# Performance work log

Hardware: AMD Instinct MI355X
Metric: run time of the kernel (lower is better)

Reference implementation:

```python
import jax, jax.numpy as jnp
import numpy as np

N, E, D, H, OUT = 50000, 640000, 128, 128, 32


def setup_inputs() -> dict:
    key = jax.random.key(0)
    ks = jax.random.split(key, 12)
    s = 0.02
    return {
        "x": jax.random.normal(ks[0], (N, D), dtype=jnp.float32),
        "edge_src": jax.random.randint(ks[1], (E,), 0, N),
        "edge_dst": jax.random.randint(ks[2], (E,), 0, N),
        "Wp": jax.random.normal(ks[3], (D, H), dtype=jnp.float32) * s,
        "bp": jnp.zeros((H,), jnp.float32),
        "Wm": jax.random.normal(ks[4], (2 * H, H), dtype=jnp.float32) * s,
        "bm": jnp.zeros((H,), jnp.float32),
        "Wu": jax.random.normal(ks[5], (2 * H, H), dtype=jnp.float32) * s,
        "bu": jnp.zeros((H,), jnp.float32),
        "gamma": jnp.ones((H,), jnp.float32),
        "beta": jnp.zeros((H,), jnp.float32),
        "Wd": jax.random.normal(ks[6], (H, OUT), dtype=jnp.float32) * s,
        "bd": jnp.zeros((OUT,), jnp.float32),
    }


def reference(x, edge_src, edge_dst, Wp, bp, Wm, bm, Wu, bu, gamma, beta, Wd, bd):
    n = x.shape[0]
    h = H
    # node projection: [N, H]
    h0 = x @ Wp + bp
    # edge messages: relu(concat(h0[src], h0[dst]) @ Wm + bm), split matmul avoids concat
    msg = jax.nn.relu(h0[edge_src] @ Wm[:h] + h0[edge_dst] @ Wm[h:] + bm)  # [E, H]
    # segment-mean into target nodes
    pooled_sum = jax.ops.segment_sum(msg, edge_dst, num_segments=n)
    cnt = jax.ops.segment_sum(jnp.ones((msg.shape[0],), msg.dtype), edge_dst, num_segments=n)
    pooled = pooled_sum / jnp.maximum(cnt, 1.0)[:, None]  # [N, H]
    # residual next-state: relu(h0 + Dense(concat(h0, pooled)))
    upd = h0 @ Wu[:h] + pooled @ Wu[h:] + bu
    hn = jax.nn.relu(h0 + upd)
    # layer norm over feature axis
    mu = jnp.mean(hn, axis=-1, keepdims=True)
    var = jnp.mean(jnp.square(hn - mu), axis=-1, keepdims=True)
    hn = (hn - mu) * jax.lax.rsqrt(var + 1e-6) * gamma + beta
    # graph-level mean pool -> [1, H] -> [1, OUT]
    g = jnp.mean(hn, axis=0, keepdims=True)
    return g @ Wd + bd
```

## Files before the change

kernel.cpp:

```cpp
#include <hip/hip_runtime.h>

#define N_NODES 50000
#define N_EDGES 640000
#define HD 128
#define TILE_N 128
#define NSCB 196

typedef short bf16x8 __attribute__((ext_vector_type(8)));
typedef float f32x4 __attribute__((ext_vector_type(4)));
typedef unsigned short u16x8 __attribute__((ext_vector_type(8)));
typedef unsigned short u16x4 __attribute__((ext_vector_type(4)));

__device__ __forceinline__ unsigned short f2bf(float f) {
  unsigned u = __float_as_uint(f);
  return (unsigned short)((u + 0x7fffu + ((u >> 16) & 1u)) >> 16);
}
__device__ __forceinline__ float bf2f(unsigned short h) {
  return __uint_as_float(((unsigned)h) << 16);
}
__device__ __forceinline__ int swzb(int row, int u) {
  return row * 256 + ((u ^ (row & 7)) << 4);
}

__device__ __forceinline__ void load_A(const char* Ash, int lane, int wr, bf16x8 A[4][4]) {
  const int l15 = lane & 15, l4 = lane >> 4;
#pragma unroll
  for (int rt = 0; rt < 4; ++rt)
#pragma unroll
    for (int kk = 0; kk < 4; ++kk)
      A[rt][kk] = *(const bf16x8*)(Ash + swzb(wr * 64 + rt * 16 + l15, kk * 4 + l4));
}

__device__ __forceinline__ void mfma_AB(const bf16x8 A[4][4], const char* Bsh,
                                        int lane, int wc, f32x4 acc[4][4]) {
  const int l15 = lane & 15, l4 = lane >> 4;
#pragma unroll
  for (int ct = 0; ct < 4; ++ct) {
    bf16x8 B[4];
#pragma unroll
    for (int kk = 0; kk < 4; ++kk)
      B[kk] = *(const bf16x8*)(Bsh + swzb(wc * 64 + ct * 16 + l15, kk * 4 + l4));
#pragma unroll
    for (int rt = 0; rt < 4; ++rt)
#pragma unroll
      for (int kk = 0; kk < 4; ++kk)
        acc[rt][ct] =
            __builtin_amdgcn_mfma_f32_16x16x32_bf16(A[rt][kk], B[kk], acc[rt][ct], 0, 0, 0);
  }
}

__device__ __forceinline__ void scatter_acc(char* Tsh, int lane, int wr, int wc,
                                            const f32x4 acc[4][4]) {
  const int l15 = lane & 15, l4 = lane >> 4;
#pragma unroll
  for (int rt = 0; rt < 4; ++rt)
#pragma unroll
    for (int ct = 0; ct < 4; ++ct) {
      int c = wc * 64 + ct * 16 + l15;
#pragma unroll
      for (int e = 0; e < 4; ++e) {
        int r = wr * 64 + rt * 16 + l4 * 4 + e;
        *(unsigned short*)(Tsh + swzb(r, c >> 3) + (c & 7) * 2) = f2bf(acc[rt][ct][e]);
      }
    }
}

__device__ __forceinline__ void copy_out(const char* Tsh, unsigned short* __restrict__ g,
                                         int bnode0, int tid) {
#pragma unroll
  for (int c = 0; c < 8; ++c) {
    int ul = c * 256 + tid;
    int row = ul >> 4, u = ul & 15;
    if (bnode0 + row < N_NODES)
      *(u16x8*)(g + (size_t)(bnode0 + row) * HD + u * 8) = *(const u16x8*)(Tsh + swzb(row, u));
  }
}

__device__ __forceinline__ void stage_bf(const unsigned short* __restrict__ src, char* Tsh,
                                         int bnode0, int tid, bool guard) {
#pragma unroll
  for (int c = 0; c < 8; ++c) {
    int ul = c * 256 + tid;
    int row = ul >> 4, u = ul & 15;
    u16x8 v = {0, 0, 0, 0, 0, 0, 0, 0};
    if (!guard || (bnode0 + row < N_NODES))
      v = *(const u16x8*)(src + (size_t)(bnode0 + row) * HD + u * 8);
    *(u16x8*)(Tsh + swzb(row, u)) = v;
  }
}

__device__ __forceinline__ void stage_xf(const float* __restrict__ src, char* Tsh,
                                         int bnode0, int tid) {
#pragma unroll
  for (int c = 0; c < 16; ++c) {
    int f4 = c * 256 + tid;
    int row = f4 >> 5, c4 = f4 & 31;
    float4 v = make_float4(0.f, 0.f, 0.f, 0.f);
    if (bnode0 + row < N_NODES) v = ((const float4*)src)[(size_t)(bnode0 + row) * 32 + c4];
    u16x4 p;
    p[0] = f2bf(v.x); p[1] = f2bf(v.y); p[2] = f2bf(v.z); p[3] = f2bf(v.w);
    *(u16x4*)(Tsh + swzb(row, c4 >> 1) + (c4 & 1) * 8) = p;
  }
}

__global__ __launch_bounds__(128) void k_prew(const float* __restrict__ Wp,
                                              const float* __restrict__ Wm,
                                              const float* __restrict__ Wu,
                                              unsigned short* __restrict__ WT) {
  const int s = blockIdx.x;
  const float* src = (s == 0) ? Wp : (s == 1) ? Wm : (s == 2) ? (Wm + HD * HD)
                     : (s == 3) ? Wu : (Wu + HD * HD);
  const int n = threadIdx.x;
  unsigned short* dst = WT + (size_t)s * HD * HD + (size_t)n * HD;
  for (int kc = 0; kc < HD; kc += 8) {
    u16x8 p;
#pragma unroll
    for (int j = 0; j < 8; ++j) p[j] = f2bf(src[(size_t)(kc + j) * HD + n]);
    *(u16x8*)(dst + kc) = p;
  }
}

__global__ __launch_bounds__(256, 2) void k_proj(
    const float* __restrict__ x, const unsigned short* __restrict__ WT,
    const float* __restrict__ bp, const float* __restrict__ bm,
    unsigned short* __restrict__ h0, unsigned short* __restrict__ a,
    unsigned short* __restrict__ b) {
  __shared__ char Ssh[32768];
  __shared__ char Wsh[32768];
  const int tid = threadIdx.x, lane = tid & 63, wid = tid >> 6;
  const int wr = wid >> 1, wc = wid & 1, l15 = lane & 15;
  const int bnode0 = blockIdx.x * TILE_N;

  stage_xf(x, Ssh, bnode0, tid);
  stage_bf(WT, Wsh, 0, tid, false);
  __syncthreads();

  bf16x8 A[4][4];
  f32x4 acc[4][4];
  load_A(Ssh, lane, wr, A);
#pragma unroll
  for (int ct = 0; ct < 4; ++ct) {
    float bv = bp[wc * 64 + ct * 16 + l15];
    f32x4 sv = {bv, bv, bv, bv};
#pragma unroll
    for (int rt = 0; rt < 4; ++rt) acc[rt][ct] = sv;
  }
  mfma_AB(A, Wsh, lane, wc, acc);
  __syncthreads();
  scatter_acc(Ssh, lane, wr, wc, acc);
  stage_bf(WT + 1 * HD * HD, Wsh, 0, tid, false);
  __syncthreads();
  copy_out(Ssh, h0, bnode0, tid);
  load_A(Ssh, lane, wr, A);
#pragma unroll
  for (int ct = 0; ct < 4; ++ct) {
    f32x4 z = {0.f, 0.f, 0.f, 0.f};
#pragma unroll
    for (int rt = 0; rt < 4; ++rt) acc[rt][ct] = z;
  }
  mfma_AB(A, Wsh, lane, wc, acc);
  __syncthreads();
  scatter_acc(Ssh, lane, wr, wc, acc);
  stage_bf(WT + 2 * HD * HD, Wsh, 0, tid, false);
  __syncthreads();
  copy_out(Ssh, a, bnode0, tid);
#pragma unroll
  for (int ct = 0; ct < 4; ++ct) {
    float bv = bm[wc * 64 + ct * 16 + l15];
    f32x4 sv = {bv, bv, bv, bv};
#pragma unroll
    for (int rt = 0; rt < 4; ++rt) acc[rt][ct] = sv;
  }
  mfma_AB(A, Wsh, lane, wc, acc);
  __syncthreads();
  scatter_acc(Ssh, lane, wr, wc, acc);
  __syncthreads();
  copy_out(Ssh, b, bnode0, tid);
}

__global__ void k_hist(const int* __restrict__ dst, int* __restrict__ deg,
                       int* __restrict__ pos_e) {
  int e = blockIdx.x * 256 + threadIdx.x;
  if (e < N_EDGES) pos_e[e] = atomicAdd(&deg[dst[e]], 1);
}

__global__ __launch_bounds__(256) void k_scan1(const int* __restrict__ deg,
                                               int* __restrict__ bsum) {
  __shared__ int sh[256];
  int i = blockIdx.x * 256 + threadIdx.x;
  sh[threadIdx.x] = (i < N_NODES) ? deg[i] : 0;
  __syncthreads();
  for (int off = 128; off > 0; off >>= 1) {
    if (threadIdx.x < off) sh[threadIdx.x] += sh[threadIdx.x + off];
    __syncthreads();
  }
  if (threadIdx.x == 0) bsum[blockIdx.x] = sh[0];
}

__global__ __launch_bounds__(256) void k_scan2(const int* __restrict__ bsum,
                                               int* __restrict__ boff,
                                               int* __restrict__ row_start) {
  __shared__ int sh[256];
  int t = threadIdx.x;
  int v = (t < NSCB) ? bsum[t] : 0;
  sh[t] = v;
  __syncthreads();
  for (int off = 1; off < 256; off <<= 1) {
    int add = (t >= off) ? sh[t - off] : 0;
    __syncthreads();
    sh[t] += add;
    __syncthreads();
  }
  if (t < NSCB) boff[t] = sh[t] - v;
  if (t == 255) row_start[N_NODES] = sh[255];
}

__global__ __launch_bounds__(256) void k_scan3(const int* __restrict__ deg,
                                               const int* __restrict__ boff,
                                               int* __restrict__ row_start) {
  __shared__ int sh[256];
  int t = threadIdx.x;
  int i = blockIdx.x * 256 + t;
  int v = (i < N_NODES) ? deg[i] : 0;
  sh[t] = v;
  __syncthreads();
  for (int off = 1; off < 256; off <<= 1) {
    int add = (t >= off) ? sh[t - off] : 0;
    __syncthreads();
    sh[t] += add;
    __syncthreads();
  }
  if (i < N_NODES) row_start[i] = boff[blockIdx.x] + sh[t] - v;
}

__global__ void k_scatter(const int* __restrict__ src, const int* __restrict__ dst,
                          const int* __restrict__ pos_e, const int* __restrict__ row_start,
                          int* __restrict__ es) {
  int e = blockIdx.x * 256 + threadIdx.x;
  if (e < N_EDGES) {
    int d = dst[e];
    es[row_start[d] + pos_e[e]] = src[e];
  }
}

__global__ __launch_bounds__(256) void k_agg(const unsigned short* __restrict__ a,
                                             const unsigned short* __restrict__ b,
                                             const int* __restrict__ es,
                                             const int* __restrict__ row_start,
                                             unsigned short* __restrict__ pooled) {
  const int node = blockIdx.x * 4 + (threadIdx.x >> 6);
  const int lane = threadIdx.x & 63;
  const int s = row_start[node];
  const int e = row_start[node + 1];
  const unsigned bu = ((const unsigned*)(b + (size_t)node * HD))[lane];
  const float bx = bf2f((unsigned short)(bu & 0xffffu));
  const float by = bf2f((unsigned short)(bu >> 16));
  float ax = 0.f, ay = 0.f;
  int i = s;
  for (; i + 8 <= e; i += 8) {
    unsigned av[8];
#pragma unroll
    for (int j = 0; j < 8; ++j)
      av[j] = ((const unsigned*)(a + (size_t)es[i + j] * HD))[lane];
#pragma unroll
    for (int j = 0; j < 8; ++j) {
      ax += fmaxf(bf2f((unsigned short)(av[j] & 0xffffu)) + bx, 0.f);
      ay += fmaxf(bf2f((unsigned short)(av[j] >> 16)) + by, 0.f);
    }
  }
  for (; i + 4 <= e; i += 4) {
    unsigned av[4];
#pragma unroll
    for (int j = 0; j < 4; ++j)
      av[j] = ((const unsigned*)(a + (size_t)es[i + j] * HD))[lane];
#pragma unroll
    for (int j = 0; j < 4; ++j) {
      ax += fmaxf(bf2f((unsigned short)(av[j] & 0xffffu)) + bx, 0.f);
      ay += fmaxf(bf2f((unsigned short)(av[j] >> 16)) + by, 0.f);
    }
  }
  for (; i < e; ++i) {
    unsigned a0 = ((const unsigned*)(a + (size_t)es[i] * HD))[lane];
    ax += fmaxf(bf2f((unsigned short)(a0 & 0xffffu)) + bx, 0.f);
    ay += fmaxf(bf2f((unsigned short)(a0 >> 16)) + by, 0.f);
  }
  const float inv = 1.f / fmaxf((float)(e - s), 1.f);
  unsigned o = (unsigned)f2bf(ax * inv) | ((unsigned)f2bf(ay * inv) << 16);
  ((unsigned*)(pooled + (size_t)node * HD))[lane] = o;
}

__global__ __launch_bounds__(256, 2) void k_upd(
    const unsigned short* __restrict__ h0, const unsigned short* __restrict__ pooled,
    const unsigned short* __restrict__ WT, const float* __restrict__ bu,
    const float* __restrict__ gamma, const float* __restrict__ beta,
    float* __restrict__ gsum) {
  __shared__ char Ssh[32768];
  __shared__ char Wsh[32768];
  const int tid = threadIdx.x, lane = tid & 63, wid = tid >> 6;
  const int wr = wid >> 1, wc = wid & 1, l15 = lane & 15, l4 = lane >> 4;
  const int bnode0 = blockIdx.x * TILE_N;

  stage_bf(pooled, Ssh, bnode0, tid, true);
  stage_bf(WT + 4 * HD * HD, Wsh, 0, tid, false);
  __syncthreads();

  bf16x8 A[4][4];
  f32x4 acc[4][4];
  load_A(Ssh, lane, wr, A);
#pragma unroll
  for (int ct = 0; ct < 4; ++ct) {
    float bv = bu[wc * 64 + ct * 16 + l15];
    f32x4 sv = {bv, bv, bv, bv};
#pragma unroll
    for (int rt = 0; rt < 4; ++rt) acc[rt][ct] = sv;
  }
  mfma_AB(A, Wsh, lane, wc, acc);
  __syncthreads();
  stage_bf(h0, Ssh, bnode0, tid, true);
  stage_bf(WT + 3 * HD * HD, Wsh, 0, tid, false);
  __syncthreads();
  load_A(Ssh, lane, wr, A);
  mfma_AB(A, Wsh, lane, wc, acc);
  __syncthreads();

  float rsum[4][4], rsq[4][4];
#pragma unroll
  for (int rt = 0; rt < 4; ++rt)
#pragma unroll
    for (int e = 0; e < 4; ++e) {
      int r = wr * 64 + rt * 16 + l4 * 4 + e;
      float srow = 0.f, qrow = 0.f;
#pragma unroll
      for (int ct = 0; ct < 4; ++ct) {
        int c = wc * 64 + ct * 16 + l15;
        float hv = bf2f(*(const unsigned short*)(Ssh + swzb(r, c >> 3) + (c & 7) * 2));
        float v = fmaxf(hv + acc[rt][ct][e], 0.f);
        acc[rt][ct][e] = v;
        srow += v;
        qrow += v * v;
      }
#pragma unroll
      for (int m = 1; m < 16; m <<= 1) {
        srow += __shfl_xor(srow, m);
        qrow += __shfl_xor(qrow, m);
      }
      rsum[rt][e] = srow;
      rsq[rt][e] = qrow;
    }
  float* pS = (float*)Wsh;
  float* pQ = (float*)(Wsh + 1024);
  if (l15 == 0) {
#pragma unroll
    for (int rt = 0; rt < 4; ++rt)
#pragma unroll
      for (int e = 0; e < 4; ++e) {
        int r = wr * 64 + rt * 16 + l4 * 4 + e;
        pS[r * 2 + wc] = rsum[rt][e];
        pQ[r * 2 + wc] = rsq[rt][e];
      }
  }
  __syncthreads();

  float g4[4], b4[4];
#pragma unroll
  for (int ct = 0; ct < 4; ++ct) {
    int c = wc * 64 + ct * 16 + l15;
    g4[ct] = gamma[c];
    b4[ct] = beta[c];
  }
  float gp[4] = {0.f, 0.f, 0.f, 0.f};
#pragma unroll
  for (int rt = 0; rt < 4; ++rt)
#pragma unroll
    for (int e = 0; e < 4; ++e) {
      int r = wr * 64 + rt * 16 + l4 * 4 + e;
      float s = pS[r * 2] + pS[r * 2 + 1];
      float q = pQ[r * 2] + pQ[r * 2 + 1];
      float mu = s * (1.f / 128.f);
      float var = q * (1.f / 128.f) - mu * mu;
      float rs = rsqrtf(var + 1e-6f);
      bool valid = (bnode0 + r) < N_NODES;
#pragma unroll
      for (int ct = 0; ct < 4; ++ct) {
        float v = (acc[rt][ct][e] - mu) * rs * g4[ct] + b4[ct];
        if (valid) gp[ct] += v;
      }
    }
#pragma unroll
  for (int ct = 0; ct < 4; ++ct) {
    gp[ct] += __shfl_xor(gp[ct], 16);
    gp[ct] += __shfl_xor(gp[ct], 32);
  }
  if (lane < 16) {
#pragma unroll
    for (int ct = 0; ct < 4; ++ct) atomicAdd(&gsum[wc * 64 + ct * 16 + lane], gp[ct]);
  }
}

__global__ void k_final(const float* __restrict__ gsum, const float* __restrict__ Wd,
                        const float* __restrict__ bd, float* __restrict__ out) {
  int o = threadIdx.x;
  if (o < 32) {
    float acc = bd[o];
    const float invN = 1.f / (float)N_NODES;
    for (int d = 0; d < HD; ++d) acc = fmaf(gsum[d] * invN, Wd[d * 32 + o], acc);
    out[o] = acc;
  }
}

extern "C" void kernel_launch(void* const* d_in, const int* in_sizes, int n_in,
                              void* d_out, int out_size, void* d_ws, size_t ws_size,
                              hipStream_t stream) {
  (void)in_sizes; (void)n_in; (void)out_size; (void)ws_size;
  const float* x    = (const float*)d_in[0];
  const int* esrc   = (const int*)d_in[1];
  const int* edst   = (const int*)d_in[2];
  const float* Wp   = (const float*)d_in[3];
  const float* bp   = (const float*)d_in[4];
  const float* Wm   = (const float*)d_in[5];
  const float* bm   = (const float*)d_in[6];
  const float* Wu   = (const float*)d_in[7];
  const float* bu   = (const float*)d_in[8];
  const float* gam  = (const float*)d_in[9];
  const float* bet  = (const float*)d_in[10];
  const float* Wd   = (const float*)d_in[11];
  const float* bd   = (const float*)d_in[12];
  float* out = (float*)d_out;

  char* ws = (char*)d_ws;
  size_t off = 0;
  unsigned short* WT     = (unsigned short*)(ws + off); off += 5 * (size_t)HD * HD * 2;
  unsigned short* h0     = (unsigned short*)(ws + off); off += (size_t)N_NODES * HD * 2;
  unsigned short* a      = (unsigned short*)(ws + off); off += (size_t)N_NODES * HD * 2;
  unsigned short* b      = (unsigned short*)(ws + off); off += (size_t)N_NODES * HD * 2;
  unsigned short* pooled = (unsigned short*)(ws + off); off += (size_t)N_NODES * HD * 2;
  int* es        = (int*)(ws + off);   off += (size_t)N_EDGES * 4;
  int* pos_e     = (int*)(ws + off);   off += (size_t)N_EDGES * 4;
  int* deg       = (int*)(ws + off);   off += (size_t)N_NODES * 4;
  float* gsum    = (float*)(ws + off); off += 128 * 4;
  int* row_start = (int*)(ws + off);   off += (size_t)(N_NODES + 1) * 4;
  int* bsum      = (int*)(ws + off);   off += (size_t)NSCB * 4;
  int* boff      = (int*)(ws + off);   off += (size_t)NSCB * 4;

  hipMemsetAsync(deg, 0, (size_t)(N_NODES + 128) * 4, stream);
  k_prew<<<5, 128, 0, stream>>>(Wp, Wm, Wu, WT);
  k_proj<<<(N_NODES + TILE_N - 1) / TILE_N, 256, 0, stream>>>(x, WT, bp, bm, h0, a, b);
  k_hist<<<(N_EDGES + 255) / 256, 256, 0, stream>>>(edst, deg, pos_e);
  k_scan1<<<NSCB, 256, 0, stream>>>(deg, bsum);
  k_scan2<<<1, 256, 0, stream>>>(bsum, boff, row_start);
  k_scan3<<<NSCB, 256, 0, stream>>>(deg, boff, row_start);
  k_scatter<<<(N_EDGES + 255) / 256, 256, 0, stream>>>(esrc, edst, pos_e, row_start, es);
  k_agg<<<N_NODES / 4, 256, 0, stream>>>(a, b, es, row_start, pooled);
  k_upd<<<(N_NODES + TILE_N - 1) / TILE_N, 256, 0, stream>>>(h0, pooled, WT, bu, gam, bet, gsum);
  k_final<<<1, 64, 0, stream>>>(gsum, Wd, bd, out);
}
```

Measured before the change: 222.3 us.

## Fuse neighbor aggregation into update kernel and fold final dense into last block

Gathers and mean-pools edge messages straight into shared memory inside the update kernel, which removes the pooled buffer's global round trip and one launch. The final small dense layer now runs in whichever block finishes last, detected with an atomic counter, and the memset is folded into the weight-prep kernel by adding zeroing blocks. The cost is parallelism in aggregation: each block now handles 128 nodes with 4 waves, one node per wave at a time, against 12500 small blocks before. That may hurt latency hiding for the random gathers.

```diff
diff --git a/kernel.cpp b/kernel.cpp
--- a/kernel.cpp
+++ b/kernel.cpp
@@ -5,6 +5,7 @@
 #define HD 128
 #define TILE_N 128
 #define NSCB 196
+#define NTILE 391
 
 typedef short bf16x8 __attribute__((ext_vector_type(8)));
 typedef float f32x4 __attribute__((ext_vector_type(4)));
@@ -106,7 +107,13 @@
 __global__ __launch_bounds__(128) void k_prew(const float* __restrict__ Wp,
                                               const float* __restrict__ Wm,
                                               const float* __restrict__ Wu,
-                                              unsigned short* __restrict__ WT) {
+                                              unsigned short* __restrict__ WT,
+                                              int* __restrict__ zbase) {
+  if (blockIdx.x >= 5) {
+    int idx = (blockIdx.x - 5) * 512 + threadIdx.x * 4;
+    *(int4*)(zbase + idx) = make_int4(0, 0, 0, 0);
+    return;
+  }
   const int s = blockIdx.x;
   const float* src = (s == 0) ? Wp : (s == 1) ? Wm : (s == 2) ? (Wm + HD * HD)
                      : (s == 3) ? Wu : (Wu + HD * HD);
@@ -243,65 +250,63 @@
   }
 }
 
-__global__ __launch_bounds__(256) void k_agg(const unsigned short* __restrict__ a,
-                                             const unsigned short* __restrict__ b,
-                                             const int* __restrict__ es,
-                                             const int* __restrict__ row_start,
-                                             unsigned short* __restrict__ pooled) {
-  const int node = blockIdx.x * 4 + (threadIdx.x >> 6);
-  const int lane = threadIdx.x & 63;
-  const int s = row_start[node];
-  const int e = row_start[node + 1];
-  const unsigned bu = ((const unsigned*)(b + (size_t)node * HD))[lane];
-  const float bx = bf2f((unsigned short)(bu & 0xffffu));
-  const float by = bf2f((unsigned short)(bu >> 16));
-  float ax = 0.f, ay = 0.f;
-  int i = s;
-  for (; i + 8 <= e; i += 8) {
-    unsigned av[8];
-#pragma unroll
-    for (int j = 0; j < 8; ++j)
-      av[j] = ((const unsigned*)(a + (size_t)es[i + j] * HD))[lane];
-#pragma unroll
-    for (int j = 0; j < 8; ++j) {
-      ax += fmaxf(bf2f((unsigned short)(av[j] & 0xffffu)) + bx, 0.f);
-      ay += fmaxf(bf2f((unsigned short)(av[j] >> 16)) + by, 0.f);
-    }
-  }
-  for (; i + 4 <= e; i += 4) {
-    unsigned av[4];
-#pragma unroll
-    for (int j = 0; j < 4; ++j)
-      av[j] = ((const unsigned*)(a + (size_t)es[i + j] * HD))[lane];
-#pragma unroll
-    for (int j = 0; j < 4; ++j) {
-      ax += fmaxf(bf2f((unsigned short)(av[j] & 0xffffu)) + bx, 0.f);
-      ay += fmaxf(bf2f((unsigned short)(av[j] >> 16)) + by, 0.f);
-    }
-  }
-  for (; i < e; ++i) {
-    unsigned a0 = ((const unsigned*)(a + (size_t)es[i] * HD))[lane];
-    ax += fmaxf(bf2f((unsigned short)(a0 & 0xffffu)) + bx, 0.f);
-    ay += fmaxf(bf2f((unsigned short)(a0 >> 16)) + by, 0.f);
-  }
-  const float inv = 1.f / fmaxf((float)(e - s), 1.f);
-  unsigned o = (unsigned)f2bf(ax * inv) | ((unsigned)f2bf(ay * inv) << 16);
-  ((unsigned*)(pooled + (size_t)node * HD))[lane] = o;
-}
-
-__global__ __launch_bounds__(256, 2) void k_upd(
-    const unsigned short* __restrict__ h0, const unsigned short* __restrict__ pooled,
-    const unsigned short* __restrict__ WT, const float* __restrict__ bu,
-    const float* __restrict__ gamma, const float* __restrict__ beta,
-    float* __restrict__ gsum) {
+__global__ __launch_bounds__(256, 2) void k_aggupd(
+    const unsigned short* __restrict__ h0, const unsigned short* __restrict__ a,
+    const unsigned short* __restrict__ b, const int* __restrict__ es,
+    const int* __restrict__ row_start, const unsigned short* __restrict__ WT,
+    const float* __restrict__ bu, const float* __restrict__ gamma,
+    const float* __restrict__ beta, const float* __restrict__ Wd,
+    const float* __restrict__ bd, float* __restrict__ gsum,
+    int* __restrict__ done, float* __restrict__ out) {
   __shared__ char Ssh[32768];
   __shared__ char Wsh[32768];
+  __shared__ int lastflag;
   const int tid = threadIdx.x, lane = tid & 63, wid = tid >> 6;
   const int wr = wid >> 1, wc = wid & 1, l15 = lane & 15, l4 = lane >> 4;
   const int bnode0 = blockIdx.x * TILE_N;
 
-  stage_bf(pooled, Ssh, bnode0, tid, true);
   stage_bf(WT + 4 * HD * HD, Wsh, 0, tid, false);
+  for (int rr = 0; rr < 32; ++rr) {
+    const int row = wid * 32 + rr;
+    const int n = bnode0 + row;
+    unsigned packed = 0;
+    if (n < N_NODES) {
+      const int s = row_start[n];
+      const int e = row_start[n + 1];
+      const unsigned bv = ((const unsigned*)(b + (size_t)n * HD))[lane];
+      const float bx = bf2f((unsigned short)(bv & 0xffffu));
+      const float by = bf2f((unsigned short)(bv >> 16));
+      float ax = 0.f, ay = 0.f;
+      int i = s;
+      for (; i + 8 <= e; i += 8) {
+        unsigned av[8];
+#pragma unroll
+        for (int j = 0; j < 8; ++j)
+          av[j] = ((const unsigned*)(a + (size_t)es[i + j] * HD))[lane];
+#pragma unroll
+        for (int j = 0; j < 8; ++j) {
+          ax += fmaxf(bf2f((unsigned short)(av[j] & 0xffffu)) + bx, 0.f);
+          ay += fmaxf(bf2f((unsigned short)(av[j] >> 16)) + by, 0.f);
+        }
+      }
+      for (; i + 2 <= e; i += 2) {
+        unsigned a0 = ((const unsigned*)(a + (size_t)es[i] * HD))[lane];
+        unsigned a1 = ((const unsigned*)(a + (size_t)es[i + 1] * HD))[lane];
+        ax += fmaxf(bf2f((unsigned short)(a0 & 0xffffu)) + bx, 0.f);
+        ay += fmaxf(bf2f((unsigned short)(a0 >> 16)) + by, 0.f);
+        ax += fmaxf(bf2f((unsigned short)(a1 & 0xffffu)) + bx, 0.f);
+        ay += fmaxf(bf2f((unsigned short)(a1 >> 16)) + by, 0.f);
+      }
+      for (; i < e; ++i) {
+        unsigned a0 = ((const unsigned*)(a + (size_t)es[i] * HD))[lane];
+        ax += fmaxf(bf2f((unsigned short)(a0 & 0xffffu)) + bx, 0.f);
+        ay += fmaxf(bf2f((unsigned short)(a0 >> 16)) + by, 0.f);
+      }
+      const float inv = 1.f / fmaxf((float)(e - s), 1.f);
+      packed = (unsigned)f2bf(ax * inv) | ((unsigned)f2bf(ay * inv) << 16);
+    }
+    *(unsigned*)(Ssh + swzb(row, lane >> 2) + (lane & 3) * 4) = packed;
+  }
   __syncthreads();
 
   bf16x8 A[4][4];
@@ -395,16 +400,19 @@
 #pragma unroll
     for (int ct = 0; ct < 4; ++ct) atomicAdd(&gsum[wc * 64 + ct * 16 + lane], gp[ct]);
   }
-}
-
-__global__ void k_final(const float* __restrict__ gsum, const float* __restrict__ Wd,
-                        const float* __restrict__ bd, float* __restrict__ out) {
-  int o = threadIdx.x;
-  if (o < 32) {
-    float acc = bd[o];
-    const float invN = 1.f / (float)N_NODES;
-    for (int d = 0; d < HD; ++d) acc = fmaf(gsum[d] * invN, Wd[d * 32 + o], acc);
-    out[o] = acc;
+
+  __threadfence();
+  __syncthreads();
+  if (tid == 0) lastflag = (atomicAdd(done, 1) == gridDim.x - 1) ? 1 : 0;
+  __syncthreads();
+  if (lastflag) {
+    __threadfence();
+    if (tid < 32) {
+      float acc2 = bd[tid];
+      const float invN = 1.f / (float)N_NODES;
+      for (int d = 0; d < HD; ++d) acc2 = fmaf(gsum[d] * invN, Wd[d * 32 + tid], acc2);
+      out[tid] = acc2;
+    }
   }
 }
 
@@ -429,28 +437,28 @@
 
   char* ws = (char*)d_ws;
   size_t off = 0;
-  unsigned short* WT     = (unsigned short*)(ws + off); off += 5 * (size_t)HD * HD * 2;
-  unsigned short* h0     = (unsigned short*)(ws + off); off += (size_t)N_NODES * HD * 2;
-  unsigned short* a      = (unsigned short*)(ws + off); off += (size_t)N_NODES * HD * 2;
-  unsigned short* b      = (unsigned short*)(ws + off); off += (size_t)N_NODES * HD * 2;
-  unsigned short* pooled = (unsigned short*)(ws + off); off += (size_t)N_NODES * HD * 2;
-  int* es        = (int*)(ws + off);   off += (size_t)N_EDGES * 4;
-  int* pos_e     = (int*)(ws + off);   off += (size_t)N_EDGES * 4;
-  int* deg       = (int*)(ws + off);   off += (size_t)N_NODES * 4;
-  float* gsum    = (float*)(ws + off); off += 128 * 4;
-  int* row_start = (int*)(ws + off);   off += (size_t)(N_NODES + 1) * 4;
-  int* bsum      = (int*)(ws + off);   off += (size_t)NSCB * 4;
-  int* boff      = (int*)(ws + off);   off += (size_t)NSCB * 4;
-
-  hipMemsetAsync(deg, 0, (size_t)(N_NODES + 128) * 4, stream);
-  k_prew<<<5, 128, 0, stream>>>(Wp, Wm, Wu, WT);
-  k_proj<<<(N_NODES + TILE_N - 1) / TILE_N, 256, 0, stream>>>(x, WT, bp, bm, h0, a, b);
+  unsigned short* WT = (unsigned short*)(ws + off); off += 5 * (size_t)HD * HD * 2;
+  unsigned short* h0 = (unsigned short*)(ws + off); off += (size_t)N_NODES * HD * 2;
+  unsigned short* a  = (unsigned short*)(ws + off); off += (size_t)N_NODES * HD * 2;
+  unsigned short* b  = (unsigned short*)(ws + off); off += (size_t)N_NODES * HD * 2;
+  int* es    = (int*)(ws + off); off += (size_t)N_EDGES * 4;
+  int* pos_e = (int*)(ws + off); off += (size_t)N_EDGES * 4;
+  int* zbase = (int*)(ws + off);
+  int* deg   = zbase;
+  float* gsum = (float*)(zbase + N_NODES);
+  int* done  = zbase + N_NODES + 128;
+  off += (size_t)50176 * 4;
+  int* row_start = (int*)(ws + off); off += (size_t)(N_NODES + 1) * 4;
+  int* bsum = (int*)(ws + off); off += (size_t)NSCB * 4;
+  int* boff = (int*)(ws + off); off += (size_t)NSCB * 4;
+
+  k_prew<<<103, 128, 0, stream>>>(Wp, Wm, Wu, WT, zbase);
+  k_proj<<<NTILE, 256, 0, stream>>>(x, WT, bp, bm, h0, a, b);
   k_hist<<<(N_EDGES + 255) / 256, 256, 0, stream>>>(edst, deg, pos_e);
   k_scan1<<<NSCB, 256, 0, stream>>>(deg, bsum);
   k_scan2<<<1, 256, 0, stream>>>(bsum, boff, row_start);
   k_scan3<<<NSCB, 256, 0, stream>>>(deg, boff, row_start);
   k_scatter<<<(N_EDGES + 255) / 256, 256, 0, stream>>>(esrc, edst, pos_e, row_start, es);
-  k_agg<<<N_NODES / 4, 256, 0, stream>>>(a, b, es, row_start, pooled);
-  k_upd<<<(N_NODES + TILE_N - 1) / TILE_N, 256, 0, stream>>>(h0, pooled, WT, bu, gam, bet, gsum);
-  k_final<<<1, 64, 0, stream>>>(gsum, Wd, bd, out);
-}
+  k_aggupd<<<NTILE, 256, 0, stream>>>(h0, a, b, es, row_start, WT, bu, gam, bet,
+                                      Wd, bd, gsum, done, out);
+}
```

After: 284.3 us. 27.9% more time.

## Cut kernel launches by merging memset, histogram, scans and final reduction

Applied to the files above, without the earlier changes.

Folds the workspace memset into extra blocks of the weight-prep kernel and runs the edge-degree histogram as extra blocks inside the projection kernel. It merges scan1 and scan2 through a last-block-done atomic counter, and moves the final dense readout into the last finishing block of the update kernel. The aim is to remove several small launches and their serialization gaps. In exchange it adds threadfence and atomic-counter synchronization. The histogram blocks also now compete with the projection GEMM blocks for occupancy.

```diff
diff --git a/kernel.cpp b/kernel.cpp
--- a/kernel.cpp
+++ b/kernel.cpp
@@ -5,6 +5,8 @@
 #define HD 128
 #define TILE_N 128
 #define NSCB 196
+#define NTILE 391
+#define HB 313
 
 typedef short bf16x8 __attribute__((ext_vector_type(8)));
 typedef float f32x4 __attribute__((ext_vector_type(4)));
@@ -106,7 +108,13 @@
 __global__ __launch_bounds__(128) void k_prew(const float* __restrict__ Wp,
                                               const float* __restrict__ Wm,
                                               const float* __restrict__ Wu,
-                                              unsigned short* __restrict__ WT) {
+                                              unsigned short* __restrict__ WT,
+                                              int* __restrict__ zbase) {
+  if (blockIdx.x >= 5) {
+    int idx = (blockIdx.x - 5) * 512 + threadIdx.x * 4;
+    *(int4*)(zbase + idx) = make_int4(0, 0, 0, 0);
+    return;
+  }
   const int s = blockIdx.x;
   const float* src = (s == 0) ? Wp : (s == 1) ? Wm : (s == 2) ? (Wm + HD * HD)
                      : (s == 3) ? Wu : (Wu + HD * HD);
@@ -120,16 +128,22 @@
   }
 }
 
-__global__ __launch_bounds__(256, 2) void k_proj(
+__global__ __launch_bounds__(256, 2) void k_projhist(
     const float* __restrict__ x, const unsigned short* __restrict__ WT,
     const float* __restrict__ bp, const float* __restrict__ bm,
     unsigned short* __restrict__ h0, unsigned short* __restrict__ a,
-    unsigned short* __restrict__ b) {
+    unsigned short* __restrict__ b, const int* __restrict__ edst,
+    int* __restrict__ deg, int* __restrict__ pos_e) {
   __shared__ char Ssh[32768];
   __shared__ char Wsh[32768];
+  if (blockIdx.x < HB) {
+    for (int e = blockIdx.x * 256 + threadIdx.x; e < N_EDGES; e += HB * 256)
+      pos_e[e] = atomicAdd(&deg[edst[e]], 1);
+    return;
+  }
   const int tid = threadIdx.x, lane = tid & 63, wid = tid >> 6;
   const int wr = wid >> 1, wc = wid & 1, l15 = lane & 15;
-  const int bnode0 = blockIdx.x * TILE_N;
+  const int bnode0 = (blockIdx.x - HB) * TILE_N;
 
   stage_xf(x, Ssh, bnode0, tid);
   stage_bf(WT, Wsh, 0, tid, false);
@@ -178,15 +192,13 @@
   copy_out(Ssh, b, bnode0, tid);
 }
 
-__global__ void k_hist(const int* __restrict__ dst, int* __restrict__ deg,
-                       int* __restrict__ pos_e) {
-  int e = blockIdx.x * 256 + threadIdx.x;
-  if (e < N_EDGES) pos_e[e] = atomicAdd(&deg[dst[e]], 1);
-}
-
-__global__ __launch_bounds__(256) void k_scan1(const int* __restrict__ deg,
-                                               int* __restrict__ bsum) {
+__global__ __launch_bounds__(256) void k_scan12(const int* __restrict__ deg,
+                                                int* __restrict__ bsum,
+                                                int* __restrict__ boff,
+                                                int* __restrict__ row_start,
+                                                int* __restrict__ done2) {
   __shared__ int sh[256];
+  __shared__ int amLast;
   int i = blockIdx.x * 256 + threadIdx.x;
   sh[threadIdx.x] = (i < N_NODES) ? deg[i] : 0;
   __syncthreads();
@@ -194,25 +206,27 @@
     if (threadIdx.x < off) sh[threadIdx.x] += sh[threadIdx.x + off];
     __syncthreads();
   }
-  if (threadIdx.x == 0) bsum[blockIdx.x] = sh[0];
-}
-
-__global__ __launch_bounds__(256) void k_scan2(const int* __restrict__ bsum,
-                                               int* __restrict__ boff,
-                                               int* __restrict__ row_start) {
-  __shared__ int sh[256];
-  int t = threadIdx.x;
-  int v = (t < NSCB) ? bsum[t] : 0;
-  sh[t] = v;
-  __syncthreads();
-  for (int off = 1; off < 256; off <<= 1) {
-    int add = (t >= off) ? sh[t - off] : 0;
+  if (threadIdx.x == 0) {
+    bsum[blockIdx.x] = sh[0];
+    __threadfence();
+    amLast = (atomicAdd(done2, 1) == gridDim.x - 1) ? 1 : 0;
+  }
+  __syncthreads();
+  if (amLast) {
+    __threadfence();
+    int t = threadIdx.x;
+    int v = (t < NSCB) ? bsum[t] : 0;
+    sh[t] = v;
     __syncthreads();
-    sh[t] += add;
-    __syncthreads();
-  }
-  if (t < NSCB) boff[t] = sh[t] - v;
-  if (t == 255) row_start[N_NODES] = sh[255];
+    for (int off = 1; off < 256; off <<= 1) {
+      int add = (t >= off) ? sh[t - off] : 0;
+      __syncthreads();
+      sh[t] += add;
+      __syncthreads();
+    }
+    if (t < NSCB) boff[t] = sh[t] - v;
+    if (t == 255) row_start[N_NODES] = sh[255];
+  }
 }
 
 __global__ __launch_bounds__(256) void k_scan3(const int* __restrict__ deg,
@@ -293,9 +307,11 @@
     const unsigned short* __restrict__ h0, const unsigned short* __restrict__ pooled,
     const unsigned short* __restrict__ WT, const float* __restrict__ bu,
     const float* __restrict__ gamma, const float* __restrict__ beta,
-    float* __restrict__ gsum) {
+    const float* __restrict__ Wd, const float* __restrict__ bd,
+    float* __restrict__ gsum, int* __restrict__ done, float* __restrict__ out) {
   __shared__ char Ssh[32768];
   __shared__ char Wsh[32768];
+  __shared__ int lastflag;
   const int tid = threadIdx.x, lane = tid & 63, wid = tid >> 6;
   const int wr = wid >> 1, wc = wid & 1, l15 = lane & 15, l4 = lane >> 4;
   const int bnode0 = blockIdx.x * TILE_N;
@@ -395,16 +411,19 @@
 #pragma unroll
     for (int ct = 0; ct < 4; ++ct) atomicAdd(&gsum[wc * 64 + ct * 16 + lane], gp[ct]);
   }
-}
-
-__global__ void k_final(const float* __restrict__ gsum, const float* __restrict__ Wd,
-                        const float* __restrict__ bd, float* __restrict__ out) {
-  int o = threadIdx.x;
-  if (o < 32) {
-    float acc = bd[o];
-    const float invN = 1.f / (float)N_NODES;
-    for (int d = 0; d < HD; ++d) acc = fmaf(gsum[d] * invN, Wd[d * 32 + o], acc);
-    out[o] = acc;
+
+  __threadfence();
+  __syncthreads();
+  if (tid == 0) lastflag = (atomicAdd(done, 1) == gridDim.x - 1) ? 1 : 0;
+  __syncthreads();
+  if (lastflag) {
+    __threadfence();
+    if (tid < 32) {
+      float acc2 = bd[tid];
+      const float invN = 1.f / (float)N_NODES;
+      for (int d = 0; d < HD; ++d) acc2 = fmaf(gsum[d] * invN, Wd[d * 32 + tid], acc2);
+      out[tid] = acc2;
+    }
   }
 }
 
@@ -434,23 +453,23 @@
   unsigned short* a      = (unsigned short*)(ws + off); off += (size_t)N_NODES * HD * 2;
   unsigned short* b      = (unsigned short*)(ws + off); off += (size_t)N_NODES * HD * 2;
   unsigned short* pooled = (unsigned short*)(ws + off); off += (size_t)N_NODES * HD * 2;
-  int* es        = (int*)(ws + off);   off += (size_t)N_EDGES * 4;
-  int* pos_e     = (int*)(ws + off);   off += (size_t)N_EDGES * 4;
-  int* deg       = (int*)(ws + off);   off += (size_t)N_NODES * 4;
-  float* gsum    = (float*)(ws + off); off += 128 * 4;
-  int* row_start = (int*)(ws + off);   off += (size_t)(N_NODES + 1) * 4;
-  int* bsum      = (int*)(ws + off);   off += (size_t)NSCB * 4;
-  int* boff      = (int*)(ws + off);   off += (size_t)NSCB * 4;
-
-  hipMemsetAsync(deg, 0, (size_t)(N_NODES + 128) * 4, stream);
-  k_prew<<<5, 128, 0, stream>>>(Wp, Wm, Wu, WT);
-  k_proj<<<(N_NODES + TILE_N - 1) / TILE_N, 256, 0, stream>>>(x, WT, bp, bm, h0, a, b);
-  k_hist<<<(N_EDGES + 255) / 256, 256, 0, stream>>>(edst, deg, pos_e);
-  k_scan1<<<NSCB, 256, 0, stream>>>(deg, bsum);
-  k_scan2<<<1, 256, 0, stream>>>(bsum, boff, row_start);
+  int* es    = (int*)(ws + off); off += (size_t)N_EDGES * 4;
+  int* pos_e = (int*)(ws + off); off += (size_t)N_EDGES * 4;
+  int* zbase = (int*)(ws + off);
+  int* deg   = zbase;
+  float* gsum = (float*)(zbase + N_NODES);
+  int* done  = zbase + N_NODES + 128;
+  int* done2 = zbase + N_NODES + 129;
+  off += (size_t)50176 * 4;
+  int* row_start = (int*)(ws + off); off += (size_t)(N_NODES + 1) * 4;
+  int* bsum = (int*)(ws + off); off += (size_t)NSCB * 4;
+  int* boff = (int*)(ws + off); off += (size_t)NSCB * 4;
+
+  k_prew<<<103, 128, 0, stream>>>(Wp, Wm, Wu, WT, zbase);
+  k_projhist<<<HB + NTILE, 256, 0, stream>>>(x, WT, bp, bm, h0, a, b, edst, deg, pos_e);
+  k_scan12<<<NSCB, 256, 0, stream>>>(deg, bsum, boff, row_start, done2);
   k_scan3<<<NSCB, 256, 0, stream>>>(deg, boff, row_start);
   k_scatter<<<(N_EDGES + 255) / 256, 256, 0, stream>>>(esrc, edst, pos_e, row_start, es);
   k_agg<<<N_NODES / 4, 256, 0, stream>>>(a, b, es, row_start, pooled);
-  k_upd<<<(N_NODES + TILE_N - 1) / TILE_N, 256, 0, stream>>>(h0, pooled, WT, bu, gam, bet, gsum);
-  k_final<<<1, 64, 0, stream>>>(gsum, Wd, bd, out);
-}
+  k_upd<<<NTILE, 256, 0, stream>>>(h0, pooled, WT, bu, gam, bet, Wd, bd, gsum, done, out);
+}
```

Measured after the change: 232.0 us. 4.3% more time.
